# Kernel tuning notes

Hardware: AMD Instinct MI355X
Metric: run time of the kernel (lower is better)

The kernel has to match this reference:

```python
import jax, jax.numpy as jnp
import numpy as np

B, L, K, M, N, P, D = 8, 512, 512, 64, 64, 64, 64  # M == D required for residual add


def _layernorm(x, gamma, beta, eps=1e-3):  # keras LayerNormalization default eps
    mu = jnp.mean(x, axis=-1, keepdims=True)
    var = jnp.var(x, axis=-1, keepdims=True)
    return (x - mu) * jax.lax.rsqrt(var + eps) * gamma + beta


def setup_inputs() -> dict:
    key = jax.random.key(0)
    ks = jax.random.split(key, 5)
    return {
        "q": jax.random.normal(ks[0], (B, L, D), dtype=jnp.float32),
        "k": jax.random.normal(ks[1], (B, K, D), dtype=jnp.float32),
        "vq": jax.random.normal(ks[2], (B, L, M, N), dtype=jnp.float32),
        "vk": jax.random.normal(ks[3], (B, K, P, N), dtype=jnp.float32),
        "vexp": jax.random.normal(ks[4], (B, K, P), dtype=jnp.float32),
        "scale": jnp.ones((), dtype=jnp.float32),      # keras Attention use_scale param (init 1)
        "ln_gamma": jnp.ones((D,), dtype=jnp.float32),  # LayerNormalization gamma
        "ln_beta": jnp.zeros((D,), dtype=jnp.float32),  # LayerNormalization beta
    }


def reference(q, k, vq, vk, vexp, scale, ln_gamma, ln_beta):
    # scores: keras Attention with use_scale -> scale * q @ k^T  (B, L, K)
    scores = scale * jnp.einsum('bld,bkd->blk', q, k)
    # no mask in this call path; plain softmax over keys
    weights = jax.nn.softmax(scores, axis=-1)

    # Original value path (materializes 5D 'blkmp'):
    #   s1 = einsum('blmn,bkpn->blkmp', vq, vk)
    #   v  = einsum('blkmp,bkp->blkm', s1, vexp)
    #   out = einsum('blk,blkm->blm', weights, v)
    # Mathematically identical reassociation that never builds the 5D tensor:
    vkc = jnp.einsum('bkpn,bkp->bkn', vk, vexp)       # contract P first
    tmp = jnp.einsum('blk,bkn->bln', weights, vkc)    # softmax-weighted combine over K
    attn_out = jnp.einsum('blmn,bln->blm', vq, tmp)   # contract N -> (B, L, M)

    # BaseAttentionCell / CrossAttention: residual add + LayerNorm
    return _layernorm(q + attn_out, ln_gamma, ln_beta)
```

## Files before the change

kernel.cpp:

```cpp
#include <hip/hip_runtime.h>


__global__ __launch_bounds__(256) void vkc_kernel(const float* __restrict__ vk,
                                                  const float* __restrict__ vexp,
                                                  float* __restrict__ vkc) {
    const int wave = (blockIdx.x << 2) + (threadIdx.x >> 6);
    const int lane = threadIdx.x & 63;

    const float ve_reg = vexp[wave * 64 + lane];
    const int n0 = (lane & 15) << 2;
    const float* base = vk + (long)wave * 4096;

    float ax = 0.f, ay = 0.f, az = 0.f, aw = 0.f;
    #pragma unroll
    for (int it = 0; it < 16; ++it) {
        const int p = (lane >> 4) + (it << 2);
        const float4 v4 = *(const float4*)(base + p * 64 + n0);
        const float w = __shfl(ve_reg, p, 64);
        ax += v4.x * w; ay += v4.y * w; az += v4.z * w; aw += v4.w * w;
    }
    ax += __shfl_down(ax, 32, 64); ax += __shfl_down(ax, 16, 64);
    ay += __shfl_down(ay, 32, 64); ay += __shfl_down(ay, 16, 64);
    az += __shfl_down(az, 32, 64); az += __shfl_down(az, 16, 64);
    aw += __shfl_down(aw, 32, 64); aw += __shfl_down(aw, 16, 64);

    if ((lane & 48) == 0) {
        float4 r; r.x = ax; r.y = ay; r.z = az; r.w = aw;
        *(float4*)(vkc + wave * 64 + n0) = r;
    }
}

__device__ __forceinline__ void lds_barrier() {
    asm volatile("s_waitcnt lgkmcnt(0)" ::: "memory");
    __builtin_amdgcn_s_barrier();
}

__global__ __launch_bounds__(512) void score_out_kernel(
        const float* __restrict__ q,
        const float* __restrict__ k,
        const float* __restrict__ vkc,
        const float* __restrict__ scale_p,
        const float* __restrict__ vq,
        const float* __restrict__ gamma,
        const float* __restrict__ beta,
        float* __restrict__ out) {
    __shared__ float sc[4][512];
    __shared__ float tp[8][4][64];
    __shared__ float tmp_s[4][64];
    __shared__ float attn_s[4][64];

    const int t = threadIdx.x;
    const int wv = t >> 6;
    const int lane = t & 63;
    const int batch = blockIdx.x >> 7;
    const int l0 = (blockIdx.x & 127) << 2;

    const float scale = scale_p[0];
    const float* qbase = q + (batch * 512 + l0) * 64;

    const float qres = q[(batch * 512 + l0 + (wv & 3)) * 64 + lane];

    {
        const float4* krow = (const float4*)(k + (batch * 512 + t) * 64);
        float acc[4] = {0.f, 0.f, 0.f, 0.f};
        #pragma unroll
        for (int dc = 0; dc < 16; ++dc) {
            const float4 kv = krow[dc];
            #pragma unroll
            for (int l = 0; l < 4; ++l) {
                const float4 qv4 = ((const float4*)(qbase + l * 64))[dc];
                acc[l] += qv4.x * kv.x + qv4.y * kv.y + qv4.z * kv.z + qv4.w * kv.w;
            }
        }
        #pragma unroll
        for (int l = 0; l < 4; ++l) sc[l][t] = scale * acc[l];
    }
    lds_barrier();

    if (wv < 4) {
        float vv[8]; float mx = -1e30f;
        #pragma unroll
        for (int j = 0; j < 8; ++j) { vv[j] = sc[wv][lane + 64 * j]; mx = fmaxf(mx, vv[j]); }
        #pragma unroll
        for (int off = 32; off; off >>= 1) mx = fmaxf(mx, __shfl_xor(mx, off, 64));
        float s = 0.f;
        #pragma unroll
        for (int j = 0; j < 8; ++j) { vv[j] = __expf(vv[j] - mx); s += vv[j]; }
        #pragma unroll
        for (int off = 32; off; off >>= 1) s += __shfl_xor(s, off, 64);
        const float inv = 1.0f / s;
        #pragma unroll
        for (int j = 0; j < 8; ++j) sc[wv][lane + 64 * j] = vv[j] * inv;
    }
    lds_barrier();

    const int row = batch * 512 + l0 + (wv & 3);
    const int half = wv >> 2;
    const float* vql = vq + (long)row * 4096 + half * 2048;
    float4 v[8];
    {
        const float* vkcb = vkc + batch * 512 * 64;
        const int ksub = lane >> 4;
        const int n0 = (lane & 15) << 2;
        const int kbeg = wv << 6;
        float4 a[4];
        #pragma unroll
        for (int l = 0; l < 4; ++l) { a[l].x = 0.f; a[l].y = 0.f; a[l].z = 0.f; a[l].w = 0.f; }
        #pragma unroll
        for (int i = 0; i < 16; ++i) {
            if (i < 8) v[i] = *(const float4*)(vql + i * 256 + lane * 4);
            const int kk = kbeg + (i << 2) + ksub;
            const float4 v4 = *(const float4*)(vkcb + kk * 64 + n0);
            #pragma unroll
            for (int l = 0; l < 4; ++l) {
                const float w = sc[l][kk];
                a[l].x += w * v4.x; a[l].y += w * v4.y;
                a[l].z += w * v4.z; a[l].w += w * v4.w;
            }
        }
        #pragma unroll
        for (int l = 0; l < 4; ++l) {
            a[l].x += __shfl_down(a[l].x, 32, 64); a[l].x += __shfl_down(a[l].x, 16, 64);
            a[l].y += __shfl_down(a[l].y, 32, 64); a[l].y += __shfl_down(a[l].y, 16, 64);
            a[l].z += __shfl_down(a[l].z, 32, 64); a[l].z += __shfl_down(a[l].z, 16, 64);
            a[l].w += __shfl_down(a[l].w, 32, 64); a[l].w += __shfl_down(a[l].w, 16, 64);
        }
        if (lane < 16) {
            #pragma unroll
            for (int l = 0; l < 4; ++l)
                *(float4*)&tp[wv][l][lane << 2] = a[l];
        }
    }
    lds_barrier();

    if (t < 256) {
        const int l = t >> 6, n = t & 63;
        float s = tp[0][l][n];
        #pragma unroll
        for (int w = 1; w < 8; ++w) s += tp[w][l][n];
        tmp_s[l][n] = s;
    }
    lds_barrier();

    {
        const int n0 = (lane & 15) << 2;
        const float4 t4 = *(const float4*)&tmp_s[wv & 3][n0];

        #pragma unroll
        for (int j = 0; j < 8; ++j) {
            float part = v[j].x * t4.x + v[j].y * t4.y + v[j].z * t4.z + v[j].w * t4.w;
            part += __shfl_down(part, 8, 16);
            part += __shfl_down(part, 4, 16);
            part += __shfl_down(part, 2, 16);
            part += __shfl_down(part, 1, 16);
            if ((lane & 15) == 0)
                attn_s[wv & 3][half * 32 + j * 4 + (lane >> 4)] = part;
        }
    }
    lds_barrier();

    if (t < 256) {
        const int orow = batch * 512 + l0 + wv;
        const float x = qres + attn_s[wv][lane];
        float s1 = x, s2 = x * x;
        #pragma unroll
        for (int off = 32; off; off >>= 1) {
            s1 += __shfl_xor(s1, off, 64);
            s2 += __shfl_xor(s2, off, 64);
        }
        const float mean = s1 * (1.0f / 64.0f);
        const float var = s2 * (1.0f / 64.0f) - mean * mean;
        const float r = rsqrtf(var + 1e-3f);
        out[orow * 64 + lane] = (x - mean) * r * gamma[lane] + beta[lane];
    }
}

extern "C" void kernel_launch(void* const* d_in, const int* in_sizes, int n_in,
                              void* d_out, int out_size, void* d_ws, size_t ws_size,
                              hipStream_t stream) {
    const float* q     = (const float*)d_in[0];
    const float* k     = (const float*)d_in[1];
    const float* vq    = (const float*)d_in[2];
    const float* vk    = (const float*)d_in[3];
    const float* vexp  = (const float*)d_in[4];
    const float* scale = (const float*)d_in[5];
    const float* gamma = (const float*)d_in[6];
    const float* beta  = (const float*)d_in[7];
    float* out = (float*)d_out;

    float* vkc = (float*)d_ws;

    vkc_kernel<<<1024, 256, 0, stream>>>(vk, vexp, vkc);
    score_out_kernel<<<1024, 512, 0, stream>>>(q, k, vkc, scale, vq, gamma, beta, out);
}
```

Baseline: 176.7 us.

## Fuse vkc reduction with score/softmax and stage softmax weights through global memory

Splits the work into a different pair of kernels. The first runs the vk·vexp contraction on half of each block's waves and the QK^T scores plus softmax on the other half, then writes the softmax weights (8 MB) to workspace. The second kernel reloads those weights and does the weighted combine, vq contraction and LayerNorm. The goal is to overlap the vk streaming with score compute. The cost is an extra 8 MB global write and read, and each score thread now handles two key rows. The old path is kept as a fallback when the workspace is too small.

```diff
diff --git a/kernel.cpp b/kernel.cpp
--- a/kernel.cpp
+++ b/kernel.cpp
@@ -1,5 +1,202 @@
 #include <hip/hip_runtime.h>
 
+
+__device__ __forceinline__ void lds_barrier() {
+    asm volatile("s_waitcnt lgkmcnt(0)" ::: "memory");
+    __builtin_amdgcn_s_barrier();
+}
+
+__global__ __launch_bounds__(512) void vkc_score_kernel(
+        const float* __restrict__ q,
+        const float* __restrict__ k,
+        const float* __restrict__ vk,
+        const float* __restrict__ vexp,
+        const float* __restrict__ scale_p,
+        float* __restrict__ vkc,
+        float* __restrict__ weights_g) {
+    __shared__ float sc[4][512];
+
+    const int t = threadIdx.x;
+    const int wv = t >> 6;
+    const int lane = t & 63;
+
+    if (wv >= 4) {
+        const int unit = (blockIdx.x << 2) + (wv - 4);
+        const float ve_reg = vexp[unit * 64 + lane];
+        const int n0 = (lane & 15) << 2;
+        const float* base = vk + (long)unit * 4096;
+
+        float ax = 0.f, ay = 0.f, az = 0.f, aw = 0.f;
+        #pragma unroll
+        for (int it = 0; it < 16; ++it) {
+            const int p = (lane >> 4) + (it << 2);
+            const float4 v4 = *(const float4*)(base + p * 64 + n0);
+            const float w = __shfl(ve_reg, p, 64);
+            ax += v4.x * w; ay += v4.y * w; az += v4.z * w; aw += v4.w * w;
+        }
+        ax += __shfl_down(ax, 32, 64); ax += __shfl_down(ax, 16, 64);
+        ay += __shfl_down(ay, 32, 64); ay += __shfl_down(ay, 16, 64);
+        az += __shfl_down(az, 32, 64); az += __shfl_down(az, 16, 64);
+        aw += __shfl_down(aw, 32, 64); aw += __shfl_down(aw, 16, 64);
+
+        if ((lane & 48) == 0) {
+            float4 r; r.x = ax; r.y = ay; r.z = az; r.w = aw;
+            *(float4*)(vkc + unit * 64 + n0) = r;
+        }
+        lds_barrier();
+        return;
+    }
+
+    const int batch = blockIdx.x >> 7;
+    const int l0 = (blockIdx.x & 127) << 2;
+    const float scale = scale_p[0];
+    const float* qbase = q + (batch * 512 + l0) * 64;
+
+    #pragma unroll
+    for (int kr = 0; kr < 2; ++kr) {
+        const int krow_i = t + (kr << 8);
+        const float4* krow = (const float4*)(k + (batch * 512 + krow_i) * 64);
+        float acc[4] = {0.f, 0.f, 0.f, 0.f};
+        #pragma unroll
+        for (int dc = 0; dc < 16; ++dc) {
+            const float4 kv = krow[dc];
+            #pragma unroll
+            for (int l = 0; l < 4; ++l) {
+                const float4 qv4 = ((const float4*)(qbase + l * 64))[dc];
+                acc[l] += qv4.x * kv.x + qv4.y * kv.y + qv4.z * kv.z + qv4.w * kv.w;
+            }
+        }
+        #pragma unroll
+        for (int l = 0; l < 4; ++l) sc[l][krow_i] = scale * acc[l];
+    }
+    lds_barrier();
+
+    {
+        float vv[8]; float mx = -1e30f;
+        #pragma unroll
+        for (int j = 0; j < 8; ++j) { vv[j] = sc[wv][lane + 64 * j]; mx = fmaxf(mx, vv[j]); }
+        #pragma unroll
+        for (int off = 32; off; off >>= 1) mx = fmaxf(mx, __shfl_xor(mx, off, 64));
+        float s = 0.f;
+        #pragma unroll
+        for (int j = 0; j < 8; ++j) { vv[j] = __expf(vv[j] - mx); s += vv[j]; }
+        #pragma unroll
+        for (int off = 32; off; off >>= 1) s += __shfl_xor(s, off, 64);
+        const float inv = 1.0f / s;
+        float* wrow = weights_g + (long)(batch * 512 + l0 + wv) * 512;
+        #pragma unroll
+        for (int j = 0; j < 8; ++j) wrow[lane + 64 * j] = vv[j] * inv;
+    }
+}
+
+__global__ __launch_bounds__(512) void tmp_out_kernel(
+        const float* __restrict__ q,
+        const float* __restrict__ vkc,
+        const float* __restrict__ weights_g,
+        const float* __restrict__ vq,
+        const float* __restrict__ gamma,
+        const float* __restrict__ beta,
+        float* __restrict__ out) {
+    __shared__ float sc[4][512];
+    __shared__ float tp[8][4][64];
+    __shared__ float tmp_s[4][64];
+    __shared__ float attn_s[4][64];
+
+    const int t = threadIdx.x;
+    const int wv = t >> 6;
+    const int lane = t & 63;
+    const int batch = blockIdx.x >> 7;
+    const int l0 = (blockIdx.x & 127) << 2;
+
+    const float qres = q[(batch * 512 + l0 + (wv & 3)) * 64 + lane];
+
+    {
+        const float4 wchunk = *(const float4*)(weights_g +
+                                (long)(batch * 512 + l0) * 512 + t * 4);
+        *(float4*)(&sc[0][0] + t * 4) = wchunk;
+    }
+    lds_barrier();
+
+    const int row = batch * 512 + l0 + (wv & 3);
+    const int half = wv >> 2;
+    const float* vql = vq + (long)row * 4096 + half * 2048;
+    float4 v[8];
+    {
+        const float* vkcb = vkc + batch * 512 * 64;
+        const int ksub = lane >> 4;
+        const int n0 = (lane & 15) << 2;
+        const int kbeg = wv << 6;
+        float4 a[4];
+        #pragma unroll
+        for (int l = 0; l < 4; ++l) { a[l].x = 0.f; a[l].y = 0.f; a[l].z = 0.f; a[l].w = 0.f; }
+        #pragma unroll
+        for (int i = 0; i < 16; ++i) {
+            if (i < 8) v[i] = *(const float4*)(vql + i * 256 + lane * 4);
+            const int kk = kbeg + (i << 2) + ksub;
+            const float4 v4 = *(const float4*)(vkcb + kk * 64 + n0);
+            #pragma unroll
+            for (int l = 0; l < 4; ++l) {
+                const float w = sc[l][kk];
+                a[l].x += w * v4.x; a[l].y += w * v4.y;
+                a[l].z += w * v4.z; a[l].w += w * v4.w;
+            }
+        }
+        #pragma unroll
+        for (int l = 0; l < 4; ++l) {
+            a[l].x += __shfl_down(a[l].x, 32, 64); a[l].x += __shfl_down(a[l].x, 16, 64);
+            a[l].y += __shfl_down(a[l].y, 32, 64); a[l].y += __shfl_down(a[l].y, 16, 64);
+            a[l].z += __shfl_down(a[l].z, 32, 64); a[l].z += __shfl_down(a[l].z, 16, 64);
+            a[l].w += __shfl_down(a[l].w, 32, 64); a[l].w += __shfl_down(a[l].w, 16, 64);
+        }
+        if (lane < 16) {
+            #pragma unroll
+            for (int l = 0; l < 4; ++l)
+                *(float4*)&tp[wv][l][lane << 2] = a[l];
+        }
+    }
+    lds_barrier();
+
+    if (t < 256) {
+        const int l = t >> 6, n = t & 63;
+        float s = tp[0][l][n];
+        #pragma unroll
+        for (int w = 1; w < 8; ++w) s += tp[w][l][n];
+        tmp_s[l][n] = s;
+    }
+    lds_barrier();
+
+    {
+        const int n0 = (lane & 15) << 2;
+        const float4 t4 = *(const float4*)&tmp_s[wv & 3][n0];
+
+        #pragma unroll
+        for (int j = 0; j < 8; ++j) {
+            float part = v[j].x * t4.x + v[j].y * t4.y + v[j].z * t4.z + v[j].w * t4.w;
+            part += __shfl_down(part, 8, 16);
+            part += __shfl_down(part, 4, 16);
+            part += __shfl_down(part, 2, 16);
+            part += __shfl_down(part, 1, 16);
+            if ((lane & 15) == 0)
+                attn_s[wv & 3][half * 32 + j * 4 + (lane >> 4)] = part;
+        }
+    }
+    lds_barrier();
+
+    if (t < 256) {
+        const int orow = batch * 512 + l0 + wv;
+        const float x = qres + attn_s[wv][lane];
+        float s1 = x, s2 = x * x;
+        #pragma unroll
+        for (int off = 32; off; off >>= 1) {
+            s1 += __shfl_xor(s1, off, 64);
+            s2 += __shfl_xor(s2, off, 64);
+        }
+        const float mean = s1 * (1.0f / 64.0f);
+        const float var = s2 * (1.0f / 64.0f) - mean * mean;
+        const float r = rsqrtf(var + 1e-3f);
+        out[orow * 64 + lane] = (x - mean) * r * gamma[lane] + beta[lane];
+    }
+}
 
 __global__ __launch_bounds__(256) void vkc_kernel(const float* __restrict__ vk,
                                                   const float* __restrict__ vexp,
@@ -28,11 +225,6 @@
         float4 r; r.x = ax; r.y = ay; r.z = az; r.w = aw;
         *(float4*)(vkc + wave * 64 + n0) = r;
     }
-}
-
-__device__ __forceinline__ void lds_barrier() {
-    asm volatile("s_waitcnt lgkmcnt(0)" ::: "memory");
-    __builtin_amdgcn_s_barrier();
 }
 
 __global__ __launch_bounds__(512) void score_out_kernel(
@@ -57,7 +249,6 @@
 
     const float scale = scale_p[0];
     const float* qbase = q + (batch * 512 + l0) * 64;
-
     const float qres = q[(batch * 512 + l0 + (wv & 3)) * 64 + lane];
 
     {
@@ -189,7 +380,14 @@
     float* out = (float*)d_out;
 
     float* vkc = (float*)d_ws;
-
-    vkc_kernel<<<1024, 256, 0, stream>>>(vk, vexp, vkc);
-    score_out_kernel<<<1024, 512, 0, stream>>>(q, k, vkc, scale, vq, gamma, beta, out);
-}
+    float* weights = vkc + 8 * 512 * 64;
+
+    const size_t need = (size_t)(8 * 512 * 64 + 8 * 512 * 512) * sizeof(float);
+    if (ws_size >= need) {
+        vkc_score_kernel<<<1024, 512, 0, stream>>>(q, k, vk, vexp, scale, vkc, weights);
+        tmp_out_kernel<<<1024, 512, 0, stream>>>(q, vkc, weights, vq, gamma, beta, out);
+    } else {
+        vkc_kernel<<<1024, 256, 0, stream>>>(vk, vexp, vkc);
+        score_out_kernel<<<1024, 512, 0, stream>>>(q, k, vkc, scale, vq, gamma, beta, out);
+    }
+}
```

Result: slower. 183.7 us (+4.0%).
